# Kernel optimization log

Measured on AMD Instinct MI355X. Metric: run time of the kernel, lower is better.

Reference implementation:

```python
import jax, jax.numpy as jnp
import numpy as np

B, L, D, S = 4, 4096, 1024, 16
EPS = 1e-5  # nn.LayerNorm default


def setup_inputs() -> dict:
    key = jax.random.key(0)
    ks = jax.random.split(key, 8)
    s = 0.02
    return {
        "x_seq": jax.random.normal(ks[0], (B, L, D), jnp.float32),
        "h_prev": jnp.zeros((B, S), jnp.float32),
        "gamma": jnp.ones((D,), jnp.float32),
        "beta": jnp.zeros((D,), jnp.float32),
        "W_in": jax.random.normal(ks[1], (D, D), jnp.float32) * s,
        "b_in": jnp.zeros((D,), jnp.float32),
        "W_A": jax.random.normal(ks[2], (D, S), jnp.float32) * s,
        "b_A": jnp.zeros((S,), jnp.float32),
        "W_B": jax.random.normal(ks[3], (D, S), jnp.float32) * s,
        "b_B": jnp.zeros((S,), jnp.float32),
        "W_C": jax.random.normal(ks[4], (D, S), jnp.float32) * s,
        "b_C": jnp.zeros((S,), jnp.float32),
        "W_dt": jax.random.normal(ks[5], (D, 1), jnp.float32) * s,
        "b_dt": jnp.zeros((1,), jnp.float32),
        "W_out": jax.random.normal(ks[6], (D, D), jnp.float32) * s,
        "b_out": jnp.zeros((D,), jnp.float32),
    }


def _layernorm(x, gamma, beta):
    mu = jnp.mean(x, axis=-1, keepdims=True)
    var = jnp.mean(jnp.square(x - mu), axis=-1, keepdims=True)
    return (x - mu) * jax.lax.rsqrt(var + EPS) * gamma + beta


def reference(x_seq, h_prev, gamma, beta, W_in, b_in, W_A, b_A, W_B, b_B,
              W_C, b_C, W_dt, b_dt, W_out, b_out):
    # pre-scan projections (all batched over (B, L))
    x = _layernorm(x_seq, gamma, beta)
    x = jax.nn.silu(x @ W_in + b_in)                    # (B, L, D)
    log_A = -jax.nn.softplus(x @ W_A + b_A)             # (B, L, S)
    B_t = x @ W_B + b_B                                 # (B, L, S)
    C_t = x @ W_C + b_C                                 # (B, L, S)
    dt = jax.nn.softplus(x @ W_dt + b_dt)               # (B, L, 1)
    A_disc = jnp.exp(log_A * dt)                        # (B, L, S)
    u = jnp.mean(x, axis=-1, keepdims=True)             # (B, L, 1)
    Bu = (B_t * dt) * u                                 # (B, L, S)

    # selective scan: h_t = A_t * h_{t-1} + Bu_t  over time axis
    def step(h, inp):
        a_t, bu_t = inp
        h = a_t * h + bu_t
        return h, h

    h_final, hs = jax.lax.scan(
        step, h_prev,
        (jnp.swapaxes(A_disc, 0, 1), jnp.swapaxes(Bu, 0, 1)))
    hs = jnp.swapaxes(hs, 0, 1)                         # (B, L, S)

    y = jnp.sum(C_t * hs, axis=-1, keepdims=True)       # (B, L, 1)
    y_seq = (x * y) @ W_out + b_out + x_seq             # (B, L, D)
    return y_seq, h_final
```

## Files before the change

### kernel.cpp

```cpp
#include <hip/hip_runtime.h>

typedef unsigned short u16;
typedef unsigned int u32;
typedef __attribute__((ext_vector_type(8))) short short8;
typedef __attribute__((ext_vector_type(4))) float f32x4;

#define B_ 4
#define L_ 4096
#define D_ 1024
#define S_ 16
#define M_ (B_ * L_)
#define NBG 64
#define LC 64

__device__ __forceinline__ float b2f(u16 h) {
    unsigned u = ((unsigned)h) << 16;
    return __builtin_bit_cast(float, u);
}
__device__ __forceinline__ u16 f2b(float f) {
    unsigned u = __builtin_bit_cast(unsigned, f);
    u += 0x7fffu + ((u >> 16) & 1u);
    return (u16)(u >> 16);
}
__device__ __forceinline__ float softplus_f(float z) {
    return z > 20.f ? z : log1pf(__expf(z));
}
__device__ __forceinline__ void gload16(const u16* g, const u16* l) {
    __builtin_amdgcn_global_load_lds(
        (const __attribute__((address_space(1))) u32*)g,
        (__attribute__((address_space(3))) u32*)l, 16, 0, 0);
}

__global__ __launch_bounds__(256) void ln_prep_kernel(
    const float* __restrict__ x, const float* __restrict__ gamma,
    const float* __restrict__ beta, u16* __restrict__ xout,
    const float* __restrict__ W0, u16* __restrict__ Wt0,
    const float* __restrict__ W1, u16* __restrict__ Wt1,
    const float* __restrict__ WA, const float* __restrict__ WB,
    const float* __restrict__ WC, const float* __restrict__ Wdt,
    u16* __restrict__ Wp) {
    int blk = blockIdx.x, tid = threadIdx.x;
    if (blk < M_ / 4) {
        int w = tid >> 6, lane = tid & 63;
        int row = blk * 4 + w;
        const float* xr = &x[(size_t)row * D_];
        float4 v[4];
        float s = 0.f, q = 0.f;
#pragma unroll
        for (int i = 0; i < 4; i++) {
            v[i] = *(const float4*)&xr[(i * 64 + lane) * 4];
            s += v[i].x + v[i].y + v[i].z + v[i].w;
            q += v[i].x * v[i].x + v[i].y * v[i].y + v[i].z * v[i].z + v[i].w * v[i].w;
        }
#pragma unroll
        for (int o = 32; o > 0; o >>= 1) {
            s += __shfl_xor(s, o);
            q += __shfl_xor(q, o);
        }
        float mu = s * (1.f / D_);
        float rs = rsqrtf(q * (1.f / D_) - mu * mu + 1e-5f);
        u16* orow = &xout[(size_t)row * D_];
#pragma unroll
        for (int i = 0; i < 4; i++) {
            const float4 gv = *(const float4*)&gamma[(i * 64 + lane) * 4];
            const float4 bv = *(const float4*)&beta[(i * 64 + lane) * 4];
            ushort4 o4;
            o4.x = f2b((v[i].x - mu) * rs * gv.x + bv.x);
            o4.y = f2b((v[i].y - mu) * rs * gv.y + bv.y);
            o4.z = f2b((v[i].z - mu) * rs * gv.z + bv.z);
            o4.w = f2b((v[i].w - mu) * rs * gv.w + bv.w);
            *(ushort4*)&orow[(i * 64 + lane) * 4] = o4;
        }
    } else if (blk < M_ / 4 + 2048) {
        int b = blk - M_ / 4;
        const float* W = (b >> 10) ? W1 : W0;
        u16* Wt = (b >> 10) ? Wt1 : Wt0;
        int by = (b >> 5) & 31, bx = b & 31;
        int xx = tid & 31, ty = tid >> 5;
        __shared__ float t[32][33];
        for (int j = ty; j < 32; j += 8)
            t[j][xx] = W[(size_t)(by * 32 + j) * D_ + bx * 32 + xx];
        __syncthreads();
        for (int j = ty; j < 32; j += 8)
            Wt[(size_t)(bx * 32 + j) * D_ + by * 32 + xx] = f2b(t[xx][j]);
    } else {
        int idx = (blk - M_ / 4 - 2048) * 256 + tid;
        int s = idx >> 10, k = idx & 1023;
        float v;
        if (s < 16)       v = WA[k * 16 + s];
        else if (s < 32)  v = WB[k * 16 + (s - 16)];
        else if (s < 48)  v = WC[k * 16 + (s - 32)];
        else if (s == 48) v = Wdt[k];
        else if (s == 49) v = 1.0f / 1024.0f;
        else              v = 0.f;
        Wp[idx] = f2b(v);
    }
}

template <int EPI>
__global__ __launch_bounds__(512, 1) void gemm256(
    const u16* __restrict__ A, const u16* __restrict__ Bt,
    const float* __restrict__ bias, const float* __restrict__ resid,
    const float* __restrict__ yrow,
    u16* __restrict__ outB, float* __restrict__ outF,
    int M, int N, int K, int nTileN) {
    __shared__ u16 sm[65536];
    const int TILES = K >> 6;

    int nwg = gridDim.x;
    int bid = blockIdx.x;
    int swz = (bid & 7) * (nwg >> 3) + (bid >> 3);
    int bx = swz % nTileN, by = swz / nTileN;
    int rowBase = by * 256, colBase = bx * 256;

    int tid = threadIdx.x;
    int lane = tid & 63, w = tid >> 6;
    int wr = w >> 2, wc = w & 3;
    int lr = lane & 15, lg = lane >> 4;
    const unsigned woff = (unsigned)((lr * 32 + lg * 8) ^ ((lr & 8) ? 16 : 0));

    int sub = w;
    int pos = sub >> 1;
    int kblk = sub & 1;
    int r = lane >> 2;
    int chunk = (lane & 3) ^ ((r & 8) ? 2 : 0);
    int rowoff = (pos & 1) * 16 + (pos >> 1) * 128;
    const u16* gAs = A  + (size_t)(rowBase + rowoff + r) * K + kblk * 32 + chunk * 8;
    const u16* gBs = Bt + (size_t)(colBase + rowoff + r) * K + kblk * 32 + chunk * 8;
    const unsigned subb = (unsigned)sub * 512u;

#define STAGEPAIR(tau, p)                                                        \
    do {                                                                         \
        unsigned _bb = (unsigned)((tau) & 1) * 32768u;                           \
        size_t _go = (size_t)(p) * 32 * K + (size_t)(tau) * 64;                  \
        gload16(gBs + _go, &sm[_bb + 16384u + (unsigned)(p) * 4096u + subb]);    \
        gload16(gAs + _go, &sm[_bb + (unsigned)(p) * 4096u + subb]);             \
    } while (0)

    f32x4 acc[8][4] = {};

    STAGEPAIR(0, 0); STAGEPAIR(0, 1); STAGEPAIR(0, 2); STAGEPAIR(0, 3);
    if (TILES > 1) { STAGEPAIR(1, 0); STAGEPAIR(1, 1); STAGEPAIR(1, 2); }
    asm volatile("s_waitcnt vmcnt(6)" ::: "memory");
    __builtin_amdgcn_s_barrier();

    for (int t = 0; t < TILES; ++t) {
        const unsigned bb = (unsigned)(t & 1) * 32768u;
        short8 bfr[4][2], afr[2][2];
        if (t + 1 < TILES) STAGEPAIR(t + 1, 3);
#pragma unroll
        for (int n = 0; n < 4; n++) {
            int rb = wc * 4 + n;
            unsigned bo = bb + 16384u + (unsigned)(((rb & 7) >> 1)) * 4096u
                        + (unsigned)(((rb & 1) + ((rb >> 3) << 1)) << 1) * 512u + woff;
            bfr[n][0] = *(const short8*)&sm[bo];
            bfr[n][1] = *(const short8*)&sm[bo + 512u];
        }
#pragma unroll
        for (int dm = 0; dm < 2; dm++) {
            unsigned ao = bb + (unsigned)((dm + (wr << 1)) << 1) * 512u + woff;
            afr[dm][0] = *(const short8*)&sm[ao];
            afr[dm][1] = *(const short8*)&sm[ao + 512u];
        }
        __builtin_amdgcn_s_barrier();
        __builtin_amdgcn_s_setprio(1);
#pragma unroll
        for (int dm = 0; dm < 2; dm++)
#pragma unroll
            for (int n = 0; n < 4; n++)
#pragma unroll
                for (int ks = 0; ks < 2; ks++)
                    acc[dm][n] = __builtin_amdgcn_mfma_f32_16x16x32_bf16(
                        afr[dm][ks], bfr[n][ks], acc[dm][n], 0, 0, 0);
        __builtin_amdgcn_s_setprio(0);
        __builtin_amdgcn_s_barrier();
#pragma unroll
        for (int q = 1; q < 4; q++) {
            if (t + 2 < TILES) STAGEPAIR(t + 2, q - 1);
#pragma unroll
            for (int dm = 0; dm < 2; dm++) {
                int m = q * 2 + dm;
                unsigned ao = bb + (unsigned)q * 4096u
                            + (unsigned)(((m & 1) + (wr << 1)) << 1) * 512u + woff;
                afr[dm][0] = *(const short8*)&sm[ao];
                afr[dm][1] = *(const short8*)&sm[ao + 512u];
            }
            __builtin_amdgcn_s_barrier();
            __builtin_amdgcn_s_setprio(1);
#pragma unroll
            for (int dm = 0; dm < 2; dm++)
#pragma unroll
                for (int n = 0; n < 4; n++)
#pragma unroll
                    for (int ks = 0; ks < 2; ks++)
                        acc[q * 2 + dm][n] = __builtin_amdgcn_mfma_f32_16x16x32_bf16(
                            afr[dm][ks], bfr[n][ks], acc[q * 2 + dm][n], 0, 0, 0);
            __builtin_amdgcn_s_setprio(0);
            if (q == 3) {
                if (t + 2 < TILES)      asm volatile("s_waitcnt vmcnt(6)" ::: "memory");
                else if (t + 1 < TILES) asm volatile("s_waitcnt vmcnt(0)" ::: "memory");
            }
            __builtin_amdgcn_s_barrier();
        }
    }
#undef STAGEPAIR

    if (EPI == 1) {
        float bcol[4];
#pragma unroll
        for (int n = 0; n < 4; n++) bcol[n] = bias[colBase + wc * 64 + n * 16 + lr];
#pragma unroll
        for (int m = 0; m < 8; m++)
#pragma unroll
            for (int n = 0; n < 4; n++)
#pragma unroll
                for (int j = 0; j < 4; j++) {
                    int row = wr * 128 + m * 16 + lg * 4 + j;
                    int col = wc * 64 + n * 16 + lr;
                    float v = acc[m][n][j] + bcol[n];
                    v = v / (1.f + __expf(-v));
                    int cbs = (col >> 4) ^ lg;
                    sm[row * 256 + cbs * 16 + (col & 15)] = f2b(v);
                }
        __syncthreads();
        int rr = tid >> 1, half = tid & 1;
        u16* gout = outB + (size_t)(rowBase + rr) * N + colBase;
#pragma unroll
        for (int q = 0; q < 8; q++) {
            int cb = half * 8 + q;
            int cbs = cb ^ ((rr >> 2) & 3);
            *(uint4*)&gout[cb * 16] = *(const uint4*)&sm[rr * 256 + cbs * 16];
        }
    } else {
        float bcol[4];
#pragma unroll
        for (int n = 0; n < 4; n++) bcol[n] = bias[colBase + wc * 64 + n * 16 + lr];
#pragma unroll
        for (int m = 0; m < 8; m++) {
            float yr[4];
#pragma unroll
            for (int j = 0; j < 4; j++)
                yr[j] = yrow[rowBase + wr * 128 + m * 16 + lg * 4 + j];
#pragma unroll
            for (int n = 0; n < 4; n++)
#pragma unroll
                for (int j = 0; j < 4; j++) {
                    int row = rowBase + wr * 128 + m * 16 + lg * 4 + j;
                    int col = colBase + wc * 64 + n * 16 + lr;
                    size_t o = (size_t)row * N + col;
                    outF[o] = acc[m][n][j] * yr[j] + bcol[n] + resid[o];
                }
        }
    }
}

__global__ __launch_bounds__(256) void proj_kernel(
    const u16* __restrict__ X, const u16* __restrict__ Wp,
    const float* __restrict__ bA, const float* __restrict__ bB,
    const float* __restrict__ bC, const float* __restrict__ bdt,
    float* __restrict__ Ad, float* __restrict__ Bu, float* __restrict__ Ct,
    float* __restrict__ Pb, float* __restrict__ Qb) {
    __shared__ u16 Xs[2][64][32];
    __shared__ u16 Ws[2][64][32];
    __shared__ float Psh[64][17], Qsh[64][17];
    int rowBase = blockIdx.x * 64;
    int tid = threadIdx.x, lane = tid & 63, w = tid >> 6;
    int lr = lane & 15, lg = lane >> 4;
    f32x4 acc[4] = {};
    const int sr = lane >> 2, sc = (lane & 3) * 8;
    const u16* gX = &X[(size_t)(rowBase + w * 16 + sr) * 1024 + sc];
    const u16* gW = &Wp[(size_t)(w * 16 + sr) * 1024 + sc];

#define PSTAGE(d, k0)                              \
    do {                                           \
        gload16(gX + (k0), &Xs[d][w * 16][0]);     \
        gload16(gW + (k0), &Ws[d][w * 16][0]);     \
    } while (0)

    PSTAGE(0, 0);
    __syncthreads();
    int cur = 0;
    for (int k0 = 0; k0 < 1024; k0 += 32) {
        if (k0 + 32 < 1024) PSTAGE(cur ^ 1, k0 + 32);
        short8 a = *(const short8*)&Xs[cur][w * 16 + lr][lg * 8];
#pragma unroll
        for (int n = 0; n < 4; n++) {
            short8 b = *(const short8*)&Ws[cur][n * 16 + lr][lg * 8];
            acc[n] = __builtin_amdgcn_mfma_f32_16x16x32_bf16(a, b, acc[n], 0, 0, 0);
        }
        __syncthreads();
        cur ^= 1;
    }
#undef PSTAGE
    float bdt0 = bdt[0];
#pragma unroll
    for (int j = 0; j < 4; j++) {
        int rl = w * 16 + lg * 4 + j;
        int row = rowBase + rl;
        float dtr = __shfl(acc[3][j], lg * 16 + 0, 64);
        float uv  = __shfl(acc[3][j], lg * 16 + 1, 64);
        float dt = softplus_f(dtr + bdt0);
        float zA = acc[0][j] + bA[lr];
        float zB = acc[1][j] + bB[lr];
        float zC = acc[2][j] + bC[lr];
        size_t o = (size_t)row * 16 + lr;
        float adv = __expf(-dt * softplus_f(zA));
        float buv = zB * dt * uv;
        Ad[o] = adv;
        Bu[o] = buv;
        Ct[o] = zC;
        Psh[rl][lr] = adv;
        Qsh[rl][lr] = buv;
    }
    __syncthreads();
    if (tid < 16) {
        float P = 1.f, Q = 0.f;
        for (int rr = 0; rr < 64; rr++) {
            float pa = Psh[rr][tid];
            P = pa * P;
            Q = pa * Q + Qsh[rr][tid];
        }
        int o = blockIdx.x * S_ + tid;
        Pb[o] = P; Qb[o] = Q;
    }
}

__global__ __launch_bounds__(1024) void scan_part3(
    const float* __restrict__ Ad, const float* __restrict__ Bu,
    const float* __restrict__ Ct, const float* __restrict__ Pb,
    const float* __restrict__ Qb, const float* __restrict__ hprev,
    float* __restrict__ y, float* __restrict__ hfinal) {
    int b = blockIdx.x >> 6, g = blockIdx.x & 63;
    int tid = threadIdx.x;
    int s = tid & 15, c = tid >> 4;
    size_t idx = ((size_t)b * L_ + g * LC + c) * S_ + s;
    float a = Ad[idx], bu = Bu[idx];
    __shared__ float Ps[16][64], Qs[16][64], Hin[16][65];
    Ps[s][c] = a; Qs[s][c] = bu;
    __syncthreads();
    if (tid < 16) {
        float h = hprev[b * S_ + tid];
        for (int gg = 0; gg < g; gg++) {
            int o = (b * NBG + gg) * S_ + tid;
            h = Pb[o] * h + Qb[o];
        }
        for (int cc = 0; cc < 64; cc++) {
            Hin[tid][cc] = h;
            h = Ps[tid][cc] * h + Qs[tid][cc];
        }
        if (g == NBG - 1) hfinal[b * S_ + tid] = h;
    }
    __syncthreads();
    float h = a * Hin[s][c] + bu;
    float p = Ct[idx] * h;
    p += __shfl_xor(p, 1);
    p += __shfl_xor(p, 2);
    p += __shfl_xor(p, 4);
    p += __shfl_xor(p, 8);
    if (s == 0) y[(size_t)b * L_ + g * LC + c] = p;
}

extern "C" void kernel_launch(void* const* d_in, const int* in_sizes, int n_in,
                              void* d_out, int out_size, void* d_ws, size_t ws_size,
                              hipStream_t stream) {
    const float* x_seq  = (const float*)d_in[0];
    const float* h_prev = (const float*)d_in[1];
    const float* gamma  = (const float*)d_in[2];
    const float* beta   = (const float*)d_in[3];
    const float* W_in   = (const float*)d_in[4];
    const float* b_in   = (const float*)d_in[5];
    const float* W_A    = (const float*)d_in[6];
    const float* b_A    = (const float*)d_in[7];
    const float* W_B    = (const float*)d_in[8];
    const float* b_B    = (const float*)d_in[9];
    const float* W_C    = (const float*)d_in[10];
    const float* b_C    = (const float*)d_in[11];
    const float* W_dt   = (const float*)d_in[12];
    const float* b_dt   = (const float*)d_in[13];
    const float* W_out  = (const float*)d_in[14];
    const float* b_out  = (const float*)d_in[15];

    char* ws = (char*)d_ws;
    u16*   x_ln   = (u16*)(ws + 0);
    u16*   x      = (u16*)(ws + 33554432);
    u16*   Wt_in  = (u16*)(ws + 67108864);
    u16*   Wt_out = (u16*)(ws + 69206016);
    u16*   Wp     = (u16*)(ws + 71303168);
    float* Ad     = (float*)(ws + 71434240);
    float* Bu     = (float*)(ws + 72482816);
    float* Ct     = (float*)(ws + 73531392);
    float* yv     = (float*)(ws + 74579968);
    float* Pb     = (float*)(ws + 74645504);
    float* Qb     = (float*)(ws + 74661888);
    float* out    = (float*)d_out;

    ln_prep_kernel<<<M_ / 4 + 2048 + 256, 256, 0, stream>>>(
        x_seq, gamma, beta, x_ln,
        W_in, Wt_in, W_out, Wt_out, W_A, W_B, W_C, W_dt, Wp);
    gemm256<1><<<(M_ / 256) * (D_ / 256), 512, 0, stream>>>(
        x_ln, Wt_in, b_in, nullptr, nullptr, x, nullptr, M_, D_, D_, D_ / 256);
    proj_kernel<<<M_ / 64, 256, 0, stream>>>(x, Wp, b_A, b_B, b_C, b_dt,
                                             Ad, Bu, Ct, Pb, Qb);
    scan_part3<<<B_ * NBG, 1024, 0, stream>>>(Ad, Bu, Ct, Pb, Qb, h_prev,
                                              yv, out + (size_t)M_ * D_);
    gemm256<2><<<(M_ / 256) * (D_ / 256), 512, 0, stream>>>(
        x, Wt_out, b_out, x_seq, yv, nullptr, out, M_, D_, D_, D_ / 256);
}
```

Baseline: 148.8 us.

## Use 4 waves per GEMM block with 128x128 per-wave tiles and simpler double-buffering

Halves the GEMM workgroup from 8 to 4 waves, so each wave computes a 128x128 output tile (8x8 MFMA accumulators) and reuses its B fragments across more A rows. The fine-grained quarter-tile staged pipeline with multiple barriers per K-tile is replaced by a whole-tile prefetch into the alternate buffer, followed by a single vmcnt(0) wait and barrier. This cuts LDS reads per MFMA and barrier overhead. It roughly doubles accumulator registers per wave (256 VGPRs just for acc), which risks spills, and leaves fewer waves to hide global and LDS latency.

```diff
diff --git a/kernel.cpp b/kernel.cpp
--- a/kernel.cpp
+++ b/kernel.cpp
@@ -98,7 +98,7 @@
 }
 
 template <int EPI>
-__global__ __launch_bounds__(512, 1) void gemm256(
+__global__ __launch_bounds__(256, 1) void gemm256(
     const u16* __restrict__ A, const u16* __restrict__ Bt,
     const float* __restrict__ bias, const float* __restrict__ resid,
     const float* __restrict__ yrow,
@@ -115,126 +115,111 @@
 
     int tid = threadIdx.x;
     int lane = tid & 63, w = tid >> 6;
-    int wr = w >> 2, wc = w & 3;
+    int wr = w >> 1, wc = w & 1;
     int lr = lane & 15, lg = lane >> 4;
     const unsigned woff = (unsigned)((lr * 32 + lg * 8) ^ ((lr & 8) ? 16 : 0));
 
-    int sub = w;
-    int pos = sub >> 1;
-    int kblk = sub & 1;
+    int pos0 = w >> 1;
+    int kblk = w & 1;
     int r = lane >> 2;
     int chunk = (lane & 3) ^ ((r & 8) ? 2 : 0);
-    int rowoff = (pos & 1) * 16 + (pos >> 1) * 128;
-    const u16* gAs = A  + (size_t)(rowBase + rowoff + r) * K + kblk * 32 + chunk * 8;
-    const u16* gBs = Bt + (size_t)(colBase + rowoff + r) * K + kblk * 32 + chunk * 8;
-    const unsigned subb = (unsigned)sub * 512u;
-
-#define STAGEPAIR(tau, p)                                                        \
+    int rowoff0 = (pos0 & 1) * 16;
+    const u16* gA0 = A  + (size_t)(rowBase + rowoff0 + r) * K + kblk * 32 + chunk * 8;
+    const u16* gA1 = gA0 + (size_t)128 * K;
+    const u16* gB0 = Bt + (size_t)(colBase + rowoff0 + r) * K + kblk * 32 + chunk * 8;
+    const u16* gB1 = gB0 + (size_t)128 * K;
+    const unsigned sub0 = (unsigned)w * 512u;
+    const unsigned sub1 = (unsigned)(w + 4) * 512u;
+
+#define STAGE_ALL(sbb, tau)                                                      \
     do {                                                                         \
-        unsigned _bb = (unsigned)((tau) & 1) * 32768u;                           \
-        size_t _go = (size_t)(p) * 32 * K + (size_t)(tau) * 64;                  \
-        gload16(gBs + _go, &sm[_bb + 16384u + (unsigned)(p) * 4096u + subb]);    \
-        gload16(gAs + _go, &sm[_bb + (unsigned)(p) * 4096u + subb]);             \
+        _Pragma("unroll")                                                        \
+        for (int p = 0; p < 4; p++) {                                            \
+            size_t _go = (size_t)p * 32 * K + (size_t)(tau) * 64;                \
+            unsigned _rb = (sbb) + (unsigned)p * 4096u;                          \
+            gload16(gB0 + _go, &sm[_rb + 16384u + sub0]);                        \
+            gload16(gB1 + _go, &sm[_rb + 16384u + sub1]);                        \
+            gload16(gA0 + _go, &sm[_rb + sub0]);                                 \
+            gload16(gA1 + _go, &sm[_rb + sub1]);                                 \
+        }                                                                        \
     } while (0)
 
-    f32x4 acc[8][4] = {};
-
-    STAGEPAIR(0, 0); STAGEPAIR(0, 1); STAGEPAIR(0, 2); STAGEPAIR(0, 3);
-    if (TILES > 1) { STAGEPAIR(1, 0); STAGEPAIR(1, 1); STAGEPAIR(1, 2); }
-    asm volatile("s_waitcnt vmcnt(6)" ::: "memory");
+    f32x4 acc[8][8] = {};
+
+    STAGE_ALL(0u, 0);
+    asm volatile("s_waitcnt vmcnt(0)" ::: "memory");
     __builtin_amdgcn_s_barrier();
 
     for (int t = 0; t < TILES; ++t) {
         const unsigned bb = (unsigned)(t & 1) * 32768u;
-        short8 bfr[4][2], afr[2][2];
-        if (t + 1 < TILES) STAGEPAIR(t + 1, 3);
-#pragma unroll
-        for (int n = 0; n < 4; n++) {
-            int rb = wc * 4 + n;
-            unsigned bo = bb + 16384u + (unsigned)(((rb & 7) >> 1)) * 4096u
-                        + (unsigned)(((rb & 1) + ((rb >> 3) << 1)) << 1) * 512u + woff;
+        const unsigned nb = (unsigned)((t + 1) & 1) * 32768u;
+        if (t + 1 < TILES) STAGE_ALL(nb, t + 1);
+        short8 bfr[8][2];
+#pragma unroll
+        for (int n = 0; n < 8; n++) {
+            unsigned bo = bb + 16384u + (unsigned)(n >> 1) * 4096u
+                        + (unsigned)((n & 1) + (wc << 1)) * 1024u + woff;
             bfr[n][0] = *(const short8*)&sm[bo];
             bfr[n][1] = *(const short8*)&sm[bo + 512u];
         }
 #pragma unroll
-        for (int dm = 0; dm < 2; dm++) {
-            unsigned ao = bb + (unsigned)((dm + (wr << 1)) << 1) * 512u + woff;
-            afr[dm][0] = *(const short8*)&sm[ao];
-            afr[dm][1] = *(const short8*)&sm[ao + 512u];
-        }
-        __builtin_amdgcn_s_barrier();
-        __builtin_amdgcn_s_setprio(1);
-#pragma unroll
-        for (int dm = 0; dm < 2; dm++)
-#pragma unroll
-            for (int n = 0; n < 4; n++)
-#pragma unroll
-                for (int ks = 0; ks < 2; ks++)
-                    acc[dm][n] = __builtin_amdgcn_mfma_f32_16x16x32_bf16(
-                        afr[dm][ks], bfr[n][ks], acc[dm][n], 0, 0, 0);
-        __builtin_amdgcn_s_setprio(0);
-        __builtin_amdgcn_s_barrier();
-#pragma unroll
-        for (int q = 1; q < 4; q++) {
-            if (t + 2 < TILES) STAGEPAIR(t + 2, q - 1);
+        for (int q = 0; q < 4; q++) {
+            short8 afr[2][2];
 #pragma unroll
             for (int dm = 0; dm < 2; dm++) {
-                int m = q * 2 + dm;
                 unsigned ao = bb + (unsigned)q * 4096u
-                            + (unsigned)(((m & 1) + (wr << 1)) << 1) * 512u + woff;
+                            + (unsigned)(dm + (wr << 1)) * 1024u + woff;
                 afr[dm][0] = *(const short8*)&sm[ao];
                 afr[dm][1] = *(const short8*)&sm[ao + 512u];
             }
-            __builtin_amdgcn_s_barrier();
-            __builtin_amdgcn_s_setprio(1);
-#pragma unroll
-            for (int dm = 0; dm < 2; dm++)
-#pragma unroll
-                for (int n = 0; n < 4; n++)
-#pragma unroll
-                    for (int ks = 0; ks < 2; ks++)
+#pragma unroll
+            for (int ks = 0; ks < 2; ks++)
+#pragma unroll
+                for (int dm = 0; dm < 2; dm++)
+#pragma unroll
+                    for (int n = 0; n < 8; n++)
                         acc[q * 2 + dm][n] = __builtin_amdgcn_mfma_f32_16x16x32_bf16(
                             afr[dm][ks], bfr[n][ks], acc[q * 2 + dm][n], 0, 0, 0);
-            __builtin_amdgcn_s_setprio(0);
-            if (q == 3) {
-                if (t + 2 < TILES)      asm volatile("s_waitcnt vmcnt(6)" ::: "memory");
-                else if (t + 1 < TILES) asm volatile("s_waitcnt vmcnt(0)" ::: "memory");
-            }
-            __builtin_amdgcn_s_barrier();
-        }
-    }
-#undef STAGEPAIR
+        }
+        if (t + 1 < TILES) asm volatile("s_waitcnt vmcnt(0)" ::: "memory");
+        __builtin_amdgcn_s_barrier();
+    }
+#undef STAGE_ALL
 
     if (EPI == 1) {
-        float bcol[4];
-#pragma unroll
-        for (int n = 0; n < 4; n++) bcol[n] = bias[colBase + wc * 64 + n * 16 + lr];
+        float bcol[8];
+#pragma unroll
+        for (int n = 0; n < 8; n++) bcol[n] = bias[colBase + wc * 128 + n * 16 + lr];
 #pragma unroll
         for (int m = 0; m < 8; m++)
 #pragma unroll
-            for (int n = 0; n < 4; n++)
+            for (int n = 0; n < 8; n++)
 #pragma unroll
                 for (int j = 0; j < 4; j++) {
                     int row = wr * 128 + m * 16 + lg * 4 + j;
-                    int col = wc * 64 + n * 16 + lr;
+                    int col = wc * 128 + n * 16 + lr;
                     float v = acc[m][n][j] + bcol[n];
                     v = v / (1.f + __expf(-v));
                     int cbs = (col >> 4) ^ lg;
                     sm[row * 256 + cbs * 16 + (col & 15)] = f2b(v);
                 }
         __syncthreads();
-        int rr = tid >> 1, half = tid & 1;
-        u16* gout = outB + (size_t)(rowBase + rr) * N + colBase;
-#pragma unroll
-        for (int q = 0; q < 8; q++) {
-            int cb = half * 8 + q;
-            int cbs = cb ^ ((rr >> 2) & 3);
-            *(uint4*)&gout[cb * 16] = *(const uint4*)&sm[rr * 256 + cbs * 16];
+        int half = tid & 1;
+#pragma unroll
+        for (int rep = 0; rep < 2; rep++) {
+            int rr = rep * 128 + (tid >> 1);
+            u16* gout = outB + (size_t)(rowBase + rr) * N + colBase;
+#pragma unroll
+            for (int q = 0; q < 8; q++) {
+                int cb = half * 8 + q;
+                int cbs = cb ^ ((rr >> 2) & 3);
+                *(uint4*)&gout[cb * 16] = *(const uint4*)&sm[rr * 256 + cbs * 16];
+            }
         }
     } else {
-        float bcol[4];
-#pragma unroll
-        for (int n = 0; n < 4; n++) bcol[n] = bias[colBase + wc * 64 + n * 16 + lr];
+        float bcol[8];
+#pragma unroll
+        for (int n = 0; n < 8; n++) bcol[n] = bias[colBase + wc * 128 + n * 16 + lr];
 #pragma unroll
         for (int m = 0; m < 8; m++) {
             float yr[4];
@@ -242,11 +227,11 @@
             for (int j = 0; j < 4; j++)
                 yr[j] = yrow[rowBase + wr * 128 + m * 16 + lg * 4 + j];
 #pragma unroll
-            for (int n = 0; n < 4; n++)
+            for (int n = 0; n < 8; n++)
 #pragma unroll
                 for (int j = 0; j < 4; j++) {
                     int row = rowBase + wr * 128 + m * 16 + lg * 4 + j;
-                    int col = colBase + wc * 64 + n * 16 + lr;
+                    int col = colBase + wc * 128 + n * 16 + lr;
                     size_t o = (size_t)row * N + col;
                     outF[o] = acc[m][n][j] * yr[j] + bcol[n] + resid[o];
                 }
@@ -397,12 +382,12 @@
     ln_prep_kernel<<<M_ / 4 + 2048 + 256, 256, 0, stream>>>(
         x_seq, gamma, beta, x_ln,
         W_in, Wt_in, W_out, Wt_out, W_A, W_B, W_C, W_dt, Wp);
-    gemm256<1><<<(M_ / 256) * (D_ / 256), 512, 0, stream>>>(
+    gemm256<1><<<(M_ / 256) * (D_ / 256), 256, 0, stream>>>(
         x_ln, Wt_in, b_in, nullptr, nullptr, x, nullptr, M_, D_, D_, D_ / 256);
     proj_kernel<<<M_ / 64, 256, 0, stream>>>(x, Wp, b_A, b_B, b_C, b_dt,
                                              Ad, Bu, Ct, Pb, Qb);
     scan_part3<<<B_ * NBG, 1024, 0, stream>>>(Ad, Bu, Ct, Pb, Qb, h_prev,
                                               yv, out + (size_t)M_ * D_);
-    gemm256<2><<<(M_ / 256) * (D_ / 256), 512, 0, stream>>>(
+    gemm256<2><<<(M_ / 256) * (D_ / 256), 256, 0, stream>>>(
         x, Wt_out, b_out, x_seq, yv, nullptr, out, M_, D_, D_, D_ / 256);
 }
```

Result: slower. 165.5 us (+11.2%).
